# Kernel optimization log

Measured on AMD Instinct MI355X. Metric: run time of the kernel, lower is better.

The kernel has to match this reference:

```python
import jax, jax.numpy as jnp
import numpy as np

N, E, IN, HID, OUT = 8192, 262144, 3000, 256, 64
EPS = 1e-5


def setup_inputs() -> dict:
    key = jax.random.key(0)
    k = jax.random.split(key, 16)
    s = lambda i, shp, sc: jax.random.normal(k[i], shp, jnp.float32) * sc
    return {
        "feat": s(0, (N, IN), 1.0),
        "feat_a": s(1, (N, IN), 1.0),
        "graph_neigh": jax.random.uniform(k[2], (N, N), jnp.float32),
        "W1": s(3, (IN, HID), (1.0 / IN) ** 0.5),
        "att_src": s(4, (HID,), (1.0 / HID) ** 0.5),
        "att_dst": s(5, (HID,), (1.0 / HID) ** 0.5),
        "W2": s(6, (HID, OUT), (1.0 / HID) ** 0.5),
        "Wd1": s(7, (OUT, HID), (1.0 / OUT) ** 0.5),
        "bd1": jnp.zeros((HID,), jnp.float32),
        "gamma": jnp.ones((HID,), jnp.float32),
        "beta": jnp.zeros((HID,), jnp.float32),
        "Wd2": s(8, (HID, IN), (1.0 / HID) ** 0.5),
        "bd2": jnp.zeros((IN,), jnp.float32),
        "disc_W": s(9, (OUT, OUT), (1.0 / OUT) ** 0.5),
        "disc_b": jnp.zeros((), jnp.float32),
        "edge_index": jax.random.randint(k[10], (2, E), 0, N),
    }


def _gat_conv1(x, W1, att_src, att_dst, src, dst):
    # GATConv, heads=1, concat=False, no self-loops, no bias
    h = x @ W1                                    # [N, HID]
    a_src = h @ att_src                           # [N]
    a_dst = h @ att_dst                           # [N]
    e = jax.nn.leaky_relu(a_src[src] + a_dst[dst], 0.2)   # [E]
    m = jax.ops.segment_max(e, dst, num_segments=N)
    p = jnp.exp(e - m[dst])
    z = jax.ops.segment_sum(p, dst, num_segments=N)
    alpha = p / (z[dst] + 1e-16)                  # segment softmax over in-edges
    return jax.ops.segment_sum(alpha[:, None] * h[src], dst, num_segments=N)


def _encode(x, W1, att_src, att_dst, W2, src, dst):
    h1 = jax.nn.elu(_gat_conv1(x, W1, att_src, att_dst, src, dst))
    # conv2 is invoked with attention=False -> GraphST GATConv returns only lin(x) (heads=1 mean)
    return h1 @ W2


def _decoder(h, Wd1, bd1, gamma, beta, Wd2, bd2):
    z = h @ Wd1 + bd1
    mu = z.mean(0)
    var = z.var(0)  # biased, matches torch BN training normalization
    z = (z - mu) * jax.lax.rsqrt(var + EPS) * gamma + beta
    z = jax.nn.elu(z)
    return z @ Wd2 + bd2


def _readout(h, mask):
    vsum = mask @ h                               # [N, OUT]
    g = vsum / mask.sum(1, keepdims=True)
    g = g / jnp.clip(jnp.linalg.norm(g, axis=1, keepdims=True), 1e-12)
    return jax.nn.sigmoid(g)


def reference(feat, feat_a, graph_neigh, W1, att_src, att_dst, W2, Wd1, bd1,
              gamma, beta, Wd2, bd2, disc_W, disc_b, edge_index):
    src, dst = edge_index[0], edge_index[1]
    h2 = _encode(feat, W1, att_src, att_dst, W2, src, dst)
    h2_a = _encode(feat_a, W1, att_src, att_dst, W2, src, dst)
    h3 = _decoder(h2, Wd1, bd1, gamma, beta, Wd2, bd2)
    g = _readout(h2, graph_neigh)
    g_a = _readout(h2_a, graph_neigh)

    def disc(c, hp, hm):
        sc1 = jnp.einsum('nd,de,ne->n', hp, disc_W, c) + disc_b
        sc2 = jnp.einsum('nd,de,ne->n', hm, disc_W, c) + disc_b
        return jnp.stack([sc1, sc2], axis=1)

    ret = disc(g, h2, h2_a)
    ret_a = disc(g_a, h2_a, h2)
    return (h2, h3, ret, ret_a, h2, h2_a)
```

## Files before the change

### kernel.cpp

```cpp
#include <hip/hip_runtime.h>
#include <hip/hip_bf16.h>
#include <math.h>

constexpr int NN  = 8192;
constexpr int EE  = 262144;
constexpr int IN  = 3000;
constexpr int INP = 3008;
constexpr int HID = 256;
constexpr int OUT = 64;

constexpr long O_H2   = 0;
constexpr long O_H3   = 524288;
constexpr long O_RET  = 25100288;
constexpr long O_RETA = 25116672;
constexpr long O_H2B  = 25133056;
constexpr long O_H2A  = 25657344;

typedef __attribute__((ext_vector_type(8))) short short8v;
typedef __attribute__((ext_vector_type(4))) float f32x4;

__device__ __forceinline__ short f2bf(float f) {
    unsigned u = __float_as_uint(f);
    return (short)((u + 0x7FFF + ((u >> 16) & 1)) >> 16);
}
__device__ __forceinline__ float bf2f(unsigned short u) {
    return __uint_as_float(((unsigned)u) << 16);
}

__global__ void cvt_W1t(const float* __restrict__ W, unsigned short* __restrict__ Wt) {
    int i = blockIdx.x * 256 + threadIdx.x;
    int n = i / INP, k = i % INP;
    Wt[i] = (k < IN) ? (unsigned short)f2bf(W[(long)k * HID + n]) : 0;
}
__global__ void cvt_W2t(const float* __restrict__ W, unsigned short* __restrict__ Wt) {
    int i = blockIdx.x * 256 + threadIdx.x;
    int n = i / HID, k = i % HID;
    Wt[i] = (unsigned short)f2bf(W[(long)k * OUT + n]);
}
__global__ void cvt_Wd1t(const float* __restrict__ W, unsigned short* __restrict__ Wt) {
    int i = blockIdx.x * 256 + threadIdx.x;
    int n = i / OUT, k = i % OUT;
    Wt[i] = (unsigned short)f2bf(W[(long)k * HID + n]);
}
__global__ void cvt_Wd2t(const float* __restrict__ W, unsigned short* __restrict__ Wt) {
    int i = blockIdx.x * 256 + threadIdx.x;
    int n = i / HID, k = i % HID;
    Wt[i] = (n < IN) ? (unsigned short)f2bf(W[(long)k * IN + n]) : 0;
}

__global__ __launch_bounds__(256) void feat_gemm(const float* __restrict__ A0,
                                                 const float* __restrict__ A1,
                                                 const unsigned short* __restrict__ Bt,
                                                 float* __restrict__ Cpart) {
    __shared__ unsigned short As[128][72];
    __shared__ unsigned short Bs[128][72];
    int xb = blockIdx.x, yb = blockIdx.y;
    int pass = yb >> 6;
    int row0 = (yb & 63) * 128, col0 = xb * 128;
    const float* A = pass ? A1 : A0;
    int t = threadIdx.x, w = t >> 6, l = t & 63;
    int sr = t >> 1, sh = (t & 1) * 32;
    int wm = (w >> 1) * 64, wn = (w & 1) * 64;
    int fr = l & 15, fq = l >> 4;
    const unsigned short* Bp = Bt + (long)(col0 + sr) * INP + sh;
    const float* Arow = A + (long)(row0 + sr) * IN;

    int tb = blockIdx.z * 12;
    int ktiles = min(12, 47 - tb);

    float4  paf[8];
    short8v pb[4];
    auto loadA = [&](int k0) {
        const float* Ar = Arow + k0 + sh;
        if (k0 + 64 <= IN) {
#pragma unroll
            for (int q = 0; q < 8; ++q) paf[q] = *reinterpret_cast<const float4*>(Ar + q * 4);
        } else {
#pragma unroll
            for (int q = 0; q < 8; ++q) {
                int kb = k0 + sh + q * 4;
                float4 v;
                v.x = (kb + 0 < IN) ? Ar[q * 4 + 0] : 0.f;
                v.y = (kb + 1 < IN) ? Ar[q * 4 + 1] : 0.f;
                v.z = (kb + 2 < IN) ? Ar[q * 4 + 2] : 0.f;
                v.w = (kb + 3 < IN) ? Ar[q * 4 + 3] : 0.f;
                paf[q] = v;
            }
        }
    };
    auto loadB = [&](int k0) {
#pragma unroll
        for (int q = 0; q < 4; ++q) pb[q] = *reinterpret_cast<const short8v*>(Bp + k0 + q * 8);
    };
    loadA(tb * 64); loadB(tb * 64);

    f32x4 acc[4][4] = {};
    for (int tt = 0; tt < ktiles; ++tt) {
#pragma unroll
        for (int q = 0; q < 4; ++q) {
            float4 v0 = paf[q * 2], v1 = paf[q * 2 + 1];
            short8v s;
            s[0]=f2bf(v0.x); s[1]=f2bf(v0.y); s[2]=f2bf(v0.z); s[3]=f2bf(v0.w);
            s[4]=f2bf(v1.x); s[5]=f2bf(v1.y); s[6]=f2bf(v1.z); s[7]=f2bf(v1.w);
            *reinterpret_cast<short8v*>(&As[sr][sh + q * 8]) = s;
        }
#pragma unroll
        for (int q = 0; q < 4; ++q)
            *reinterpret_cast<short8v*>(&Bs[sr][sh + q * 8]) = pb[q];
        __syncthreads();
        if (tt + 1 < ktiles) {
            int k0 = (tb + tt + 1) * 64;
            loadA(k0); loadB(k0);
        }
#pragma unroll
        for (int kk = 0; kk < 2; ++kk) {
            short8v fa[4], fb[4];
#pragma unroll
            for (int i = 0; i < 4; ++i)
                fa[i] = *reinterpret_cast<const short8v*>(&As[wm + i * 16 + fr][kk * 32 + fq * 8]);
#pragma unroll
            for (int j = 0; j < 4; ++j)
                fb[j] = *reinterpret_cast<const short8v*>(&Bs[wn + j * 16 + fr][kk * 32 + fq * 8]);
#pragma unroll
            for (int i = 0; i < 4; ++i)
#pragma unroll
                for (int j = 0; j < 4; ++j)
                    acc[i][j] = __builtin_amdgcn_mfma_f32_16x16x32_bf16(fa[i], fb[j], acc[i][j], 0, 0, 0);
        }
        __syncthreads();
    }
    int dc = l & 15;
    long zbase = (long)blockIdx.z * 16384 * 256;
    long rbase = (long)(pass * NN + row0) * 256;
#pragma unroll
    for (int i = 0; i < 4; ++i)
#pragma unroll
        for (int j = 0; j < 4; ++j) {
            int c = col0 + wn + j * 16 + dc;
#pragma unroll
            for (int q = 0; q < 4; ++q) {
                int r = wm + i * 16 + fq * 4 + q;
                Cpart[zbase + rbase + (long)r * 256 + c] = acc[i][j][q];
            }
        }
}

__global__ void reduce_cvt4(const float* __restrict__ p, unsigned short* __restrict__ hb) {
    long i4 = ((long)blockIdx.x * 256 + threadIdx.x) * 4;
    float4 a = *reinterpret_cast<const float4*>(p + i4);
    float4 b = *reinterpret_cast<const float4*>(p + 4194304 + i4);
    float4 c = *reinterpret_cast<const float4*>(p + 8388608 + i4);
    float4 d = *reinterpret_cast<const float4*>(p + 12582912 + i4);
    ushort4 r;
    r.x = (unsigned short)f2bf(a.x + b.x + c.x + d.x);
    r.y = (unsigned short)f2bf(a.y + b.y + c.y + d.y);
    r.z = (unsigned short)f2bf(a.z + b.z + c.z + d.z);
    r.w = (unsigned short)f2bf(a.w + b.w + c.w + d.w);
    *reinterpret_cast<ushort4*>(hb + i4) = r;
}

__global__ __launch_bounds__(256) void w2_gemm(const unsigned short* __restrict__ A,
                                               const unsigned short* __restrict__ Bt,
                                               float* __restrict__ h2f,
                                               unsigned short* __restrict__ h2b,
                                               unsigned short* __restrict__ HT,
                                               float* __restrict__ out) {
    __shared__ unsigned short As[64][72];
    __shared__ unsigned short Bs[64][72];
    int t = threadIdx.x, w = t >> 6, l = t & 63;
    int row0 = blockIdx.y * 64;
    int srow = t >> 2, scol = (t & 3) * 16;
    const unsigned short* Ap = A + (long)(row0 + srow) * HID + scol;
    const unsigned short* Bp = Bt + (long)srow * HID + scol;
    int wm = (w >> 1) * 32, wn = (w & 1) * 32;
    int fr = l & 15, fq = l >> 4;

    short8v a0r, a1r, b0r, b1r;
    a0r = *reinterpret_cast<const short8v*>(Ap);
    a1r = *reinterpret_cast<const short8v*>(Ap + 8);
    b0r = *reinterpret_cast<const short8v*>(Bp);
    b1r = *reinterpret_cast<const short8v*>(Bp + 8);

    f32x4 acc[2][2] = {};
    for (int tt = 0; tt < 4; ++tt) {
        *reinterpret_cast<short8v*>(&As[srow][scol])     = a0r;
        *reinterpret_cast<short8v*>(&As[srow][scol + 8]) = a1r;
        *reinterpret_cast<short8v*>(&Bs[srow][scol])     = b0r;
        *reinterpret_cast<short8v*>(&Bs[srow][scol + 8]) = b1r;
        __syncthreads();
        if (tt + 1 < 4) {
            const unsigned short* Ap2 = Ap + (tt + 1) * 64;
            const unsigned short* Bp2 = Bp + (tt + 1) * 64;
            a0r = *reinterpret_cast<const short8v*>(Ap2);
            a1r = *reinterpret_cast<const short8v*>(Ap2 + 8);
            b0r = *reinterpret_cast<const short8v*>(Bp2);
            b1r = *reinterpret_cast<const short8v*>(Bp2 + 8);
        }
#pragma unroll
        for (int kk = 0; kk < 2; ++kk) {
            short8v fa0 = *reinterpret_cast<const short8v*>(&As[wm + fr][kk * 32 + fq * 8]);
            short8v fa1 = *reinterpret_cast<const short8v*>(&As[wm + 16 + fr][kk * 32 + fq * 8]);
            short8v fb0 = *reinterpret_cast<const short8v*>(&Bs[wn + fr][kk * 32 + fq * 8]);
            short8v fb1 = *reinterpret_cast<const short8v*>(&Bs[wn + 16 + fr][kk * 32 + fq * 8]);
            acc[0][0] = __builtin_amdgcn_mfma_f32_16x16x32_bf16(fa0, fb0, acc[0][0], 0, 0, 0);
            acc[0][1] = __builtin_amdgcn_mfma_f32_16x16x32_bf16(fa0, fb1, acc[0][1], 0, 0, 0);
            acc[1][0] = __builtin_amdgcn_mfma_f32_16x16x32_bf16(fa1, fb0, acc[1][0], 0, 0, 0);
            acc[1][1] = __builtin_amdgcn_mfma_f32_16x16x32_bf16(fa1, fb1, acc[1][1], 0, 0, 0);
        }
        __syncthreads();
    }
    int dc = l & 15;
    int pass = row0 >> 13;
#pragma unroll
    for (int i = 0; i < 2; ++i)
#pragma unroll
        for (int j = 0; j < 2; ++j) {
            int c = wn + j * 16 + dc;
#pragma unroll
            for (int q = 0; q < 4; ++q) {
                int r = row0 + wm + i * 16 + fq * 4 + q;
                int n = r & 8191;
                float v = acc[i][j][q];
                unsigned short vb = (unsigned short)f2bf(v);
                h2f[(long)pass * 524288 + (long)n * 64 + c] = v;
                if (pass == 0) {
                    out[O_H2  + (long)n * 64 + c] = v;
                    out[O_H2B + (long)n * 64 + c] = v;
                    h2b[(long)n * 64 + c] = vb;
                } else {
                    out[O_H2A + (long)n * 64 + c] = v;
                }
                HT[(long)(pass * 64 + c) * NN + n] = vb;
            }
        }
}

__global__ __launch_bounds__(256) void wd2_gemm(const unsigned short* __restrict__ A,
                                                const unsigned short* __restrict__ Bt,
                                                const float* __restrict__ bias,
                                                float* __restrict__ Cf) {
    __shared__ unsigned short As[128][72];
    __shared__ unsigned short Bs[128][72];
    int t = threadIdx.x, w = t >> 6, l = t & 63;
    int row0 = blockIdx.y * 128, col0 = blockIdx.x * 128;
    int sr = t >> 1, sh = (t & 1) * 32;
    int wm = (w >> 1) * 64, wn = (w & 1) * 64;
    int fr = l & 15, fq = l >> 4;
    const unsigned short* Ap = A  + (long)(row0 + sr) * HID + sh;
    const unsigned short* Bp = Bt + (long)(col0 + sr) * HID + sh;

    short8v pa[4], pb[4];
#pragma unroll
    for (int q = 0; q < 4; ++q) pa[q] = *reinterpret_cast<const short8v*>(Ap + q * 8);
#pragma unroll
    for (int q = 0; q < 4; ++q) pb[q] = *reinterpret_cast<const short8v*>(Bp + q * 8);

    f32x4 acc[4][4] = {};
    for (int tt = 0; tt < 4; ++tt) {
#pragma unroll
        for (int q = 0; q < 4; ++q) {
            *reinterpret_cast<short8v*>(&As[sr][sh + q * 8]) = pa[q];
            *reinterpret_cast<short8v*>(&Bs[sr][sh + q * 8]) = pb[q];
        }
        __syncthreads();
        if (tt + 1 < 4) {
            int k0 = (tt + 1) * 64;
#pragma unroll
            for (int q = 0; q < 4; ++q) pa[q] = *reinterpret_cast<const short8v*>(Ap + k0 + q * 8);
#pragma unroll
            for (int q = 0; q < 4; ++q) pb[q] = *reinterpret_cast<const short8v*>(Bp + k0 + q * 8);
        }
#pragma unroll
        for (int kk = 0; kk < 2; ++kk) {
            short8v fa[4], fb[4];
#pragma unroll
            for (int i = 0; i < 4; ++i)
                fa[i] = *reinterpret_cast<const short8v*>(&As[wm + i * 16 + fr][kk * 32 + fq * 8]);
#pragma unroll
            for (int j = 0; j < 4; ++j)
                fb[j] = *reinterpret_cast<const short8v*>(&Bs[wn + j * 16 + fr][kk * 32 + fq * 8]);
#pragma unroll
            for (int i = 0; i < 4; ++i)
#pragma unroll
                for (int j = 0; j < 4; ++j)
                    acc[i][j] = __builtin_amdgcn_mfma_f32_16x16x32_bf16(fa[i], fb[j], acc[i][j], 0, 0, 0);
        }
        __syncthreads();
    }
    int dc = l & 15;
#pragma unroll
    for (int i = 0; i < 4; ++i)
#pragma unroll
        for (int j = 0; j < 4; ++j) {
            int c = col0 + wn + j * 16 + dc;
            if (c < IN) {
                float bb = bias[c];
#pragma unroll
                for (int q = 0; q < 4; ++q) {
                    int r = row0 + wm + i * 16 + fq * 4 + q;
                    Cf[(long)r * IN + c] = acc[i][j][q] + bb;
                }
            }
        }
}

__global__ __launch_bounds__(256) void wd1_gemm(const unsigned short* __restrict__ A,
                                                const unsigned short* __restrict__ Bt,
                                                const float* __restrict__ bias,
                                                float* __restrict__ C) {
    __shared__ unsigned short As[64][72];
    __shared__ unsigned short Bs[64][72];
    int t = threadIdx.x, w = t >> 6, l = t & 63;
    int row0 = blockIdx.y * 64, col0 = blockIdx.x * 64;
    int srow = t >> 2, scol = (t & 3) * 16;
    const unsigned short* Ap = A  + (long)(row0 + srow) * OUT + scol;
    const unsigned short* Bp = Bt + (long)(col0 + srow) * OUT + scol;
    int wm = (w >> 1) * 32, wn = (w & 1) * 32;
    int fr = l & 15, fq = l >> 4;

    *reinterpret_cast<short8v*>(&As[srow][scol])     = *reinterpret_cast<const short8v*>(Ap);
    *reinterpret_cast<short8v*>(&As[srow][scol + 8]) = *reinterpret_cast<const short8v*>(Ap + 8);
    *reinterpret_cast<short8v*>(&Bs[srow][scol])     = *reinterpret_cast<const short8v*>(Bp);
    *reinterpret_cast<short8v*>(&Bs[srow][scol + 8]) = *reinterpret_cast<const short8v*>(Bp + 8);
    __syncthreads();
    f32x4 acc[2][2] = {};
#pragma unroll
    for (int kk = 0; kk < 2; ++kk) {
        short8v fa0 = *reinterpret_cast<const short8v*>(&As[wm + fr][kk * 32 + fq * 8]);
        short8v fa1 = *reinterpret_cast<const short8v*>(&As[wm + 16 + fr][kk * 32 + fq * 8]);
        short8v fb0 = *reinterpret_cast<const short8v*>(&Bs[wn + fr][kk * 32 + fq * 8]);
        short8v fb1 = *reinterpret_cast<const short8v*>(&Bs[wn + 16 + fr][kk * 32 + fq * 8]);
        acc[0][0] = __builtin_amdgcn_mfma_f32_16x16x32_bf16(fa0, fb0, acc[0][0], 0, 0, 0);
        acc[0][1] = __builtin_amdgcn_mfma_f32_16x16x32_bf16(fa0, fb1, acc[0][1], 0, 0, 0);
        acc[1][0] = __builtin_amdgcn_mfma_f32_16x16x32_bf16(fa1, fb0, acc[1][0], 0, 0, 0);
        acc[1][1] = __builtin_amdgcn_mfma_f32_16x16x32_bf16(fa1, fb1, acc[1][1], 0, 0, 0);
    }
    int dc = l & 15;
#pragma unroll
    for (int i = 0; i < 2; ++i)
#pragma unroll
        for (int j = 0; j < 2; ++j) {
            int c = col0 + wn + j * 16 + dc;
            float bb = bias[c];
#pragma unroll
            for (int q = 0; q < 4; ++q) {
                int r = row0 + wm + i * 16 + fq * 4 + q;
                C[(long)r * HID + c] = acc[i][j][q] + bb;
            }
        }
}

__global__ __launch_bounds__(256) void readout_mfma2(const float* __restrict__ gn,
                                                     const unsigned short* __restrict__ HT,
                                                     float* __restrict__ vsum_part,
                                                     float* __restrict__ rowsum_part) {
    __shared__ unsigned short As[64][72];
    __shared__ unsigned short Bs[128][72];
    __shared__ float rsacc[64][4];
    int t = threadIdx.x, w = t >> 6, l = t & 63;
    int row0 = blockIdx.x * 64;
    int kc = blockIdx.y, kbeg = kc * 2048;
    int asr = t >> 2, asc = (t & 3) * 16;
    int bsr = t >> 1, bsc = (t & 1) * 32;
    const float*          Ap = gn + (long)(row0 + asr) * NN + kbeg + asc;
    const unsigned short* Bp = HT + (long)bsr * NN + kbeg + bsc;
    int wm = (w >> 1) * 32, wn = (w & 1) * 64;
    int fr = l & 15, fq = l >> 4;

    float4  a4[4];
    short8v b8[4];
#pragma unroll
    for (int q = 0; q < 4; ++q) a4[q] = *reinterpret_cast<const float4*>(Ap + q * 4);
#pragma unroll
    for (int q = 0; q < 4; ++q) b8[q] = *reinterpret_cast<const short8v*>(Bp + q * 8);

    f32x4 acc[2][4] = {};
    float myrs = 0.f;
    for (int it = 0; it < 32; ++it) {
#pragma unroll
        for (int q = 0; q < 4; ++q) {
            float4 v = a4[q];
            ushort4 s;
            s.x = (unsigned short)f2bf(v.x);
            s.y = (unsigned short)f2bf(v.y);
            s.z = (unsigned short)f2bf(v.z);
            s.w = (unsigned short)f2bf(v.w);
            *reinterpret_cast<ushort4*>(&As[asr][asc + q * 4]) = s;
            myrs += v.x + v.y + v.z + v.w;
        }
#pragma unroll
        for (int q = 0; q < 4; ++q)
            *reinterpret_cast<short8v*>(&Bs[bsr][bsc + q * 8]) = b8[q];
        __syncthreads();
        if (it + 1 < 32) {
            const float*          Ap2 = Ap + (it + 1) * 64;
            const unsigned short* Bp2 = Bp + (it + 1) * 64;
#pragma unroll
            for (int q = 0; q < 4; ++q) a4[q] = *reinterpret_cast<const float4*>(Ap2 + q * 4);
#pragma unroll
            for (int q = 0; q < 4; ++q) b8[q] = *reinterpret_cast<const short8v*>(Bp2 + q * 8);
        }
#pragma unroll
        for (int kk = 0; kk < 2; ++kk) {
            short8v fa0 = *reinterpret_cast<const short8v*>(&As[wm + fr][kk * 32 + fq * 8]);
            short8v fa1 = *reinterpret_cast<const short8v*>(&As[wm + 16 + fr][kk * 32 + fq * 8]);
#pragma unroll
            for (int j = 0; j < 4; ++j) {
                short8v fb = *reinterpret_cast<const short8v*>(&Bs[wn + j * 16 + fr][kk * 32 + fq * 8]);
                acc[0][j] = __builtin_amdgcn_mfma_f32_16x16x32_bf16(fa0, fb, acc[0][j], 0, 0, 0);
                acc[1][j] = __builtin_amdgcn_mfma_f32_16x16x32_bf16(fa1, fb, acc[1][j], 0, 0, 0);
            }
        }
        __syncthreads();
    }
    rsacc[asr][t & 3] = myrs;
    __syncthreads();
    if (t < 64)
        rowsum_part[(long)kc * NN + row0 + t] =
            rsacc[t][0] + rsacc[t][1] + rsacc[t][2] + rsacc[t][3];
    int dc = l & 15;
#pragma unroll
    for (int i = 0; i < 2; ++i)
#pragma unroll
        for (int j = 0; j < 4; ++j) {
            int c = wn + j * 16 + dc;
#pragma unroll
            for (int q = 0; q < 4; ++q) {
                int r = row0 + wm + i * 16 + fq * 4 + q;
                vsum_part[((long)kc * NN + r) * 128 + c] = acc[i][j][q];
            }
        }
}

__global__ void deg_count(const int* __restrict__ dst, int* __restrict__ deg) {
    int i = blockIdx.x * 256 + threadIdx.x;
    if (i < EE) atomicAdd(&deg[dst[i]], 1);
}

__global__ __launch_bounds__(256) void scan_offsets(const int* __restrict__ deg,
                                                    int* __restrict__ off,
                                                    int* __restrict__ cursor) {
    __shared__ int part[256];
    int t = threadIdx.x;
    int base = t * 32;
    int local[32];
    int s = 0;
#pragma unroll
    for (int i = 0; i < 32; ++i) { local[i] = s; s += deg[base + i]; }
    part[t] = s;
    __syncthreads();
    for (int o2 = 1; o2 < 256; o2 <<= 1) {
        int v = (t >= o2) ? part[t - o2] : 0;
        __syncthreads();
        part[t] += v;
        __syncthreads();
    }
    int pre = (t == 0) ? 0 : part[t - 1];
#pragma unroll
    for (int i = 0; i < 32; ++i) {
        int v = pre + local[i];
        off[base + i] = v;
        cursor[base + i] = v;
    }
}

__global__ void scatter_edges(const int* __restrict__ src, const int* __restrict__ dst,
                              int* __restrict__ cursor, int* __restrict__ ssrc) {
    int i = blockIdx.x * 256 + threadIdx.x;
    if (i >= EE) return;
    int slot = atomicAdd(&cursor[dst[i]], 1);
    ssrc[slot] = src[i];
}

__global__ void attn_coeff_bf(const unsigned short* __restrict__ h,
                              const float* __restrict__ att_src,
                              const float* __restrict__ att_dst,
                              float* __restrict__ a_src, float* __restrict__ a_dst) {
    int wave = threadIdx.x >> 6, lane = threadIdx.x & 63;
    int n = blockIdx.x * 4 + wave;
    ushort4 hv = *reinterpret_cast<const ushort4*>(&h[(long)n * HID + lane * 4]);
    float4 vs = *reinterpret_cast<const float4*>(&att_src[lane * 4]);
    float4 vd = *reinterpret_cast<const float4*>(&att_dst[lane * 4]);
    float h0 = bf2f(hv.x), h1 = bf2f(hv.y), h2v = bf2f(hv.z), h3v = bf2f(hv.w);
    float s1 = h0 * vs.x + h1 * vs.y + h2v * vs.z + h3v * vs.w;
    float s2 = h0 * vd.x + h1 * vd.y + h2v * vd.z + h3v * vd.w;
#pragma unroll
    for (int off = 32; off > 0; off >>= 1) {
        s1 += __shfl_down(s1, off);
        s2 += __shfl_down(s2, off);
    }
    if (lane == 0) { a_src[n] = s1; a_dst[n] = s2; }
}

__global__ __launch_bounds__(256) void gat_gather(const int* __restrict__ ssrc,
                                                  const int* __restrict__ off,
                                                  const int* __restrict__ deg,
                                                  const float* __restrict__ asrc2,
                                                  const float* __restrict__ adst2,
                                                  const unsigned short* __restrict__ hb2,
                                                  unsigned short* __restrict__ gat2) {
    int wv = threadIdx.x >> 6, lane = threadIdx.x & 63;
    int d = blockIdx.x * 4 + wv;
    int pass = d >> 13, node = d & 8191;
    const float* asrc = asrc2 + pass * NN;
    const unsigned short* h = hb2 + (long)pass * NN * HID;
    int o = off[node], n = deg[node];
    float ad = adst2[d];

    float m = -INFINITY;
    for (int j = lane; j < n; j += 64) {
        float e = asrc[ssrc[o + j]] + ad;
        e = e > 0.f ? e : 0.2f * e;
        m = fmaxf(m, e);
    }
#pragma unroll
    for (int t = 32; t; t >>= 1) m = fmaxf(m, __shfl_xor(m, t));
    float z = 0.f;
    for (int j = lane; j < n; j += 64) {
        float e = asrc[ssrc[o + j]] + ad;
        e = e > 0.f ? e : 0.2f * e;
        z += expf(e - m);
    }
#pragma unroll
    for (int t = 32; t; t >>= 1) z += __shfl_xor(z, t);
    float zinv = 1.0f / (z + 1e-16f);

    float4 acc = {0.f, 0.f, 0.f, 0.f};
    int j = 0;
    for (; j + 2 <= n; j += 2) {
        int s0 = ssrc[o + j], s1 = ssrc[o + j + 1];
        const ushort4 h0 = *reinterpret_cast<const ushort4*>(&h[(long)s0 * HID + lane * 4]);
        const ushort4 h1 = *reinterpret_cast<const ushort4*>(&h[(long)s1 * HID + lane * 4]);
        float e0 = asrc[s0] + ad; e0 = e0 > 0.f ? e0 : 0.2f * e0;
        float e1 = asrc[s1] + ad; e1 = e1 > 0.f ? e1 : 0.2f * e1;
        float a0 = expf(e0 - m) * zinv;
        float a1 = expf(e1 - m) * zinv;
        acc.x += a0 * bf2f(h0.x) + a1 * bf2f(h1.x);
        acc.y += a0 * bf2f(h0.y) + a1 * bf2f(h1.y);
        acc.z += a0 * bf2f(h0.z) + a1 * bf2f(h1.z);
        acc.w += a0 * bf2f(h0.w) + a1 * bf2f(h1.w);
    }
    if (j < n) {
        int s0 = ssrc[o + j];
        const ushort4 h0 = *reinterpret_cast<const ushort4*>(&h[(long)s0 * HID + lane * 4]);
        float e0 = asrc[s0] + ad; e0 = e0 > 0.f ? e0 : 0.2f * e0;
        float a0 = expf(e0 - m) * zinv;
        acc.x += a0 * bf2f(h0.x); acc.y += a0 * bf2f(h0.y);
        acc.z += a0 * bf2f(h0.z); acc.w += a0 * bf2f(h0.w);
    }
    ushort4 r;
    r.x = (unsigned short)f2bf(acc.x > 0.f ? acc.x : expm1f(acc.x));
    r.y = (unsigned short)f2bf(acc.y > 0.f ? acc.y : expm1f(acc.y));
    r.z = (unsigned short)f2bf(acc.z > 0.f ? acc.z : expm1f(acc.z));
    r.w = (unsigned short)f2bf(acc.w > 0.f ? acc.w : expm1f(acc.w));
    *reinterpret_cast<ushort4*>(&gat2[(long)d * HID + lane * 4]) = r;
}

__global__ void bn_partial(const float* __restrict__ zd, float* __restrict__ s,
                           float* __restrict__ sq) {
    int t = threadIdx.x;
    float a = 0.f, b = 0.f;
    int r0 = blockIdx.x * 128;
    for (int r = r0; r < r0 + 128; ++r) {
        float v = zd[(long)r * HID + t];
        a += v;
        b += v * v;
    }
    atomicAdd(&s[t], a);
    atomicAdd(&sq[t], b);
}

__global__ void bn_finalize(const float* __restrict__ s, const float* __restrict__ sq,
                            const float* __restrict__ gamma, const float* __restrict__ beta,
                            float* __restrict__ scale, float* __restrict__ shift) {
    int t = threadIdx.x;
    float mean = s[t] / (float)NN;
    float var  = sq[t] / (float)NN - mean * mean;
    float sc   = gamma[t] * rsqrtf(var + 1e-5f);
    scale[t] = sc;
    shift[t] = beta[t] - mean * sc;
}

__global__ void bn_apply_elu_bf(const float* __restrict__ zd, const float* __restrict__ scale,
                                const float* __restrict__ shift, unsigned short* __restrict__ zb) {
    for (long i = (long)blockIdx.x * blockDim.x + threadIdx.x; i < (long)NN * HID;
         i += (long)gridDim.x * blockDim.x) {
        int c = (int)(i & 255);
        float v = zd[i] * scale[c] + shift[c];
        v = v > 0.f ? v : expm1f(v);
        zb[i] = (unsigned short)f2bf(v);
    }
}

__global__ void readout_disc(const float* __restrict__ vsum_part,
                             const float* __restrict__ rowsum_part,
                             const float* __restrict__ h2f,
                             const float* __restrict__ W, const float* __restrict__ b,
                             float* __restrict__ ret, float* __restrict__ reta) {
    __shared__ float gg[128];
    int r = blockIdx.x, t = threadIdx.x;
    float rs = 0.f, v = 0.f;
#pragma unroll
    for (int kc = 0; kc < 4; ++kc) {
        rs += rowsum_part[(long)kc * NN + r];
        v  += vsum_part[((long)kc * NN + r) * 128 + t];
    }
    v /= rs;
    int w = t >> 6, lane = t & 63;
    float sq = v * v;
#pragma unroll
    for (int off = 32; off > 0; off >>= 1) sq += __shfl_xor(sq, off);
    float nrm = fmaxf(sqrtf(sq), 1e-12f);
    gg[t] = 1.0f / (1.0f + expf(-(v / nrm)));
    __syncthreads();
    const float* hp_base = h2f + (w ? 524288 : 0);
    const float* hm_base = h2f + (w ? 0 : 524288);
    float u = 0.f;
#pragma unroll 8
    for (int e = 0; e < 64; ++e) u += W[lane * 64 + e] * gg[w * 64 + e];
    float hp = hp_base[(long)r * 64 + lane];
    float hm = hm_base[(long)r * 64 + lane];
    float t1 = hp * u, t2 = hm * u;
#pragma unroll
    for (int off = 32; off > 0; off >>= 1) {
        t1 += __shfl_xor(t1, off);
        t2 += __shfl_xor(t2, off);
    }
    if (lane == 0) {
        float bb = b[0];
        float* dstp = w ? reta : ret;
        dstp[r * 2]     = t1 + bb;
        dstp[r * 2 + 1] = t2 + bb;
    }
}

extern "C" void kernel_launch(void* const* d_in, const int* in_sizes, int n_in,
                              void* d_out, int out_size, void* d_ws, size_t ws_size,
                              hipStream_t stream) {
    const float* feat    = (const float*)d_in[0];
    const float* feat_a  = (const float*)d_in[1];
    const float* gneigh  = (const float*)d_in[2];
    const float* W1      = (const float*)d_in[3];
    const float* att_src = (const float*)d_in[4];
    const float* att_dst = (const float*)d_in[5];
    const float* W2      = (const float*)d_in[6];
    const float* Wd1     = (const float*)d_in[7];
    const float* bd1     = (const float*)d_in[8];
    const float* gamma   = (const float*)d_in[9];
    const float* beta    = (const float*)d_in[10];
    const float* Wd2     = (const float*)d_in[11];
    const float* bd2     = (const float*)d_in[12];
    const float* disc_W  = (const float*)d_in[13];
    const float* disc_b  = (const float*)d_in[14];
    const int*   eidx    = (const int*)d_in[15];
    const int*   src = eidx;
    const int*   dst = eidx + EE;
    float* out = (float*)d_out;

    float* w = (float*)d_ws;
    unsigned short* h_bf2  = (unsigned short*)w;
    unsigned short* gat_bf2 = (unsigned short*)(w + 2097152);
    float* zdec    = w + 4194304;
    unsigned short* zdec_bf = (unsigned short*)(zdec + 2097152);
    float* h2f     = zdec + 2097152 + 1048576;
    unsigned short* h2b = (unsigned short*)(h2f + 1048576);
    unsigned short* HT  = h2b + 524288;
    float* asrc2   = (float*)(HT + 1048576);
    float* adst2   = asrc2 + 16384;
    float* bnsum   = adst2 + 16384;
    float* bnsq    = bnsum + 256;
    float* scale   = bnsq + 256;
    float* shift   = scale + 256;
    unsigned short* W1t  = (unsigned short*)(shift + 256);
    unsigned short* W2t  = W1t + 770048;
    unsigned short* Wd1t = W2t + 16384;
    unsigned short* Wd2t = Wd1t + 16384;
    int*   ideg    = (int*)(Wd2t + 786432);
    int*   ioff    = ideg + 8192;
    int*   icur    = ioff + 8192;
    int*   issrc   = icur + 8192;
    float* part = out + O_H3;
    float* vsum_part = w;
    float* rowsum_part = zdec;

    cvt_W1t<<<3008, 256, 0, stream>>>(W1, W1t);
    cvt_W2t<<<64, 256, 0, stream>>>(W2, W2t);
    cvt_Wd1t<<<64, 256, 0, stream>>>(Wd1, Wd1t);
    cvt_Wd2t<<<3072, 256, 0, stream>>>(Wd2, Wd2t);

    hipMemsetAsync(ideg, 0, 8192 * 4, stream);
    deg_count<<<EE / 256, 256, 0, stream>>>(dst, ideg);
    scan_offsets<<<1, 256, 0, stream>>>(ideg, ioff, icur);
    scatter_edges<<<EE / 256, 256, 0, stream>>>(src, dst, icur, issrc);

    feat_gemm<<<dim3(2, 128, 4), 256, 0, stream>>>(feat, feat_a, W1t, part);
    reduce_cvt4<<<4096, 256, 0, stream>>>(part, h_bf2);
    attn_coeff_bf<<<4096, 256, 0, stream>>>(h_bf2, att_src, att_dst, asrc2, adst2);
    gat_gather<<<4096, 256, 0, stream>>>(issrc, ioff, ideg, asrc2, adst2, h_bf2, gat_bf2);
    w2_gemm<<<dim3(1, 256), 256, 0, stream>>>(gat_bf2, W2t, h2f, h2b, HT, out);

    wd1_gemm<<<dim3(4, 128), 256, 0, stream>>>(h2b, Wd1t, bd1, zdec);
    hipMemsetAsync(bnsum, 0, 512 * 4, stream);
    bn_partial<<<64, 256, 0, stream>>>(zdec, bnsum, bnsq);
    bn_finalize<<<1, 256, 0, stream>>>(bnsum, bnsq, gamma, beta, scale, shift);
    bn_apply_elu_bf<<<2048, 256, 0, stream>>>(zdec, scale, shift, zdec_bf);
    wd2_gemm<<<dim3(24, 64), 256, 0, stream>>>(zdec_bf, Wd2t, bd2, out + O_H3);

    readout_mfma2<<<dim3(128, 4), 256, 0, stream>>>(gneigh, HT, vsum_part, rowsum_part);
    readout_disc<<<8192, 128, 0, stream>>>(vsum_part, rowsum_part, h2f, disc_W, disc_b,
                                           out + O_RET, out + O_RETA);
}
```

Before: 400.0 us.

## Fuse attention coefficients into split-K reduce; widen readout split-K with bf16 partials

The split-K reduction of the first GEMM now also computes the per-node attention dot products from the fp32 sums, so the separate attention-coefficient kernel and its re-read of the bf16 features go away. The graph-neighbour readout GEMM moves from 4 to 8 K-splits so 1024 blocks launch instead of 512. Its partial sums are stored as bf16 to halve the partial-write traffic. The extra bf16 rounding of partials adds error, and the rowsum buffer must now hold 8 slices.

```diff
diff --git a/kernel.cpp b/kernel.cpp
--- a/kernel.cpp
+++ b/kernel.cpp
@@ -145,18 +145,40 @@
         }
 }
 
-__global__ void reduce_cvt4(const float* __restrict__ p, unsigned short* __restrict__ hb) {
-    long i4 = ((long)blockIdx.x * 256 + threadIdx.x) * 4;
-    float4 a = *reinterpret_cast<const float4*>(p + i4);
-    float4 b = *reinterpret_cast<const float4*>(p + 4194304 + i4);
-    float4 c = *reinterpret_cast<const float4*>(p + 8388608 + i4);
-    float4 d = *reinterpret_cast<const float4*>(p + 12582912 + i4);
+__global__ __launch_bounds__(256) void reduce_attn(const float* __restrict__ p,
+                                                   const float* __restrict__ att_src,
+                                                   const float* __restrict__ att_dst,
+                                                   unsigned short* __restrict__ hb,
+                                                   float* __restrict__ a_src,
+                                                   float* __restrict__ a_dst) {
+    int wave = threadIdx.x >> 6, lane = threadIdx.x & 63;
+    int n = blockIdx.x * 4 + wave;
+    long base = (long)n * 256 + lane * 4;
+    float4 a = *reinterpret_cast<const float4*>(p + base);
+    float4 b = *reinterpret_cast<const float4*>(p + 4194304 + base);
+    float4 c = *reinterpret_cast<const float4*>(p + 8388608 + base);
+    float4 d = *reinterpret_cast<const float4*>(p + 12582912 + base);
+    float4 hv;
+    hv.x = a.x + b.x + c.x + d.x;
+    hv.y = a.y + b.y + c.y + d.y;
+    hv.z = a.z + b.z + c.z + d.z;
+    hv.w = a.w + b.w + c.w + d.w;
     ushort4 r;
-    r.x = (unsigned short)f2bf(a.x + b.x + c.x + d.x);
-    r.y = (unsigned short)f2bf(a.y + b.y + c.y + d.y);
-    r.z = (unsigned short)f2bf(a.z + b.z + c.z + d.z);
-    r.w = (unsigned short)f2bf(a.w + b.w + c.w + d.w);
-    *reinterpret_cast<ushort4*>(hb + i4) = r;
+    r.x = (unsigned short)f2bf(hv.x);
+    r.y = (unsigned short)f2bf(hv.y);
+    r.z = (unsigned short)f2bf(hv.z);
+    r.w = (unsigned short)f2bf(hv.w);
+    *reinterpret_cast<ushort4*>(hb + base) = r;
+    float4 vs = *reinterpret_cast<const float4*>(&att_src[lane * 4]);
+    float4 vd = *reinterpret_cast<const float4*>(&att_dst[lane * 4]);
+    float s1 = hv.x * vs.x + hv.y * vs.y + hv.z * vs.z + hv.w * vs.w;
+    float s2 = hv.x * vd.x + hv.y * vd.y + hv.z * vd.z + hv.w * vd.w;
+#pragma unroll
+    for (int off = 32; off > 0; off >>= 1) {
+        s1 += __shfl_down(s1, off);
+        s2 += __shfl_down(s2, off);
+    }
+    if (lane == 0) { a_src[n] = s1; a_dst[n] = s2; }
 }
 
 __global__ __launch_bounds__(256) void w2_gemm(const unsigned short* __restrict__ A,
@@ -352,14 +374,14 @@
 
 __global__ __launch_bounds__(256) void readout_mfma2(const float* __restrict__ gn,
                                                      const unsigned short* __restrict__ HT,
-                                                     float* __restrict__ vsum_part,
+                                                     unsigned short* __restrict__ vsum_part,
                                                      float* __restrict__ rowsum_part) {
     __shared__ unsigned short As[64][72];
     __shared__ unsigned short Bs[128][72];
     __shared__ float rsacc[64][4];
     int t = threadIdx.x, w = t >> 6, l = t & 63;
     int row0 = blockIdx.x * 64;
-    int kc = blockIdx.y, kbeg = kc * 2048;
+    int kc = blockIdx.y, kbeg = kc * 1024;
     int asr = t >> 2, asc = (t & 3) * 16;
     int bsr = t >> 1, bsc = (t & 1) * 32;
     const float*          Ap = gn + (long)(row0 + asr) * NN + kbeg + asc;
@@ -376,7 +398,7 @@
 
     f32x4 acc[2][4] = {};
     float myrs = 0.f;
-    for (int it = 0; it < 32; ++it) {
+    for (int it = 0; it < 16; ++it) {
 #pragma unroll
         for (int q = 0; q < 4; ++q) {
             float4 v = a4[q];
@@ -392,7 +414,7 @@
         for (int q = 0; q < 4; ++q)
             *reinterpret_cast<short8v*>(&Bs[bsr][bsc + q * 8]) = b8[q];
         __syncthreads();
-        if (it + 1 < 32) {
+        if (it + 1 < 16) {
             const float*          Ap2 = Ap + (it + 1) * 64;
             const unsigned short* Bp2 = Bp + (it + 1) * 64;
 #pragma unroll
@@ -427,7 +449,7 @@
 #pragma unroll
             for (int q = 0; q < 4; ++q) {
                 int r = row0 + wm + i * 16 + fq * 4 + q;
-                vsum_part[((long)kc * NN + r) * 128 + c] = acc[i][j][q];
+                vsum_part[((long)kc * NN + r) * 128 + c] = (unsigned short)f2bf(acc[i][j][q]);
             }
         }
 }
@@ -470,26 +492,6 @@
     if (i >= EE) return;
     int slot = atomicAdd(&cursor[dst[i]], 1);
     ssrc[slot] = src[i];
-}
-
-__global__ void attn_coeff_bf(const unsigned short* __restrict__ h,
-                              const float* __restrict__ att_src,
-                              const float* __restrict__ att_dst,
-                              float* __restrict__ a_src, float* __restrict__ a_dst) {
-    int wave = threadIdx.x >> 6, lane = threadIdx.x & 63;
-    int n = blockIdx.x * 4 + wave;
-    ushort4 hv = *reinterpret_cast<const ushort4*>(&h[(long)n * HID + lane * 4]);
-    float4 vs = *reinterpret_cast<const float4*>(&att_src[lane * 4]);
-    float4 vd = *reinterpret_cast<const float4*>(&att_dst[lane * 4]);
-    float h0 = bf2f(hv.x), h1 = bf2f(hv.y), h2v = bf2f(hv.z), h3v = bf2f(hv.w);
-    float s1 = h0 * vs.x + h1 * vs.y + h2v * vs.z + h3v * vs.w;
-    float s2 = h0 * vd.x + h1 * vd.y + h2v * vd.z + h3v * vd.w;
-#pragma unroll
-    for (int off = 32; off > 0; off >>= 1) {
-        s1 += __shfl_down(s1, off);
-        s2 += __shfl_down(s2, off);
-    }
-    if (lane == 0) { a_src[n] = s1; a_dst[n] = s2; }
 }
 
 __global__ __launch_bounds__(256) void gat_gather(const int* __restrict__ ssrc,
@@ -592,7 +594,7 @@
     }
 }
 
-__global__ void readout_disc(const float* __restrict__ vsum_part,
+__global__ void readout_disc(const unsigned short* __restrict__ vsum_part,
                              const float* __restrict__ rowsum_part,
                              const float* __restrict__ h2f,
                              const float* __restrict__ W, const float* __restrict__ b,
@@ -601,9 +603,9 @@
     int r = blockIdx.x, t = threadIdx.x;
     float rs = 0.f, v = 0.f;
 #pragma unroll
-    for (int kc = 0; kc < 4; ++kc) {
+    for (int kc = 0; kc < 8; ++kc) {
         rs += rowsum_part[(long)kc * NN + r];
-        v  += vsum_part[((long)kc * NN + r) * 128 + t];
+        v  += bf2f(vsum_part[((long)kc * NN + r) * 128 + t]);
     }
     v /= rs;
     int w = t >> 6, lane = t & 63;
@@ -680,7 +682,7 @@
     int*   icur    = ioff + 8192;
     int*   issrc   = icur + 8192;
     float* part = out + O_H3;
-    float* vsum_part = w;
+    unsigned short* vsum_part = (unsigned short*)w;
     float* rowsum_part = zdec;
 
     cvt_W1t<<<3008, 256, 0, stream>>>(W1, W1t);
@@ -694,8 +696,7 @@
     scatter_edges<<<EE / 256, 256, 0, stream>>>(src, dst, icur, issrc);
 
     feat_gemm<<<dim3(2, 128, 4), 256, 0, stream>>>(feat, feat_a, W1t, part);
-    reduce_cvt4<<<4096, 256, 0, stream>>>(part, h_bf2);
-    attn_coeff_bf<<<4096, 256, 0, stream>>>(h_bf2, att_src, att_dst, asrc2, adst2);
+    reduce_attn<<<4096, 256, 0, stream>>>(part, att_src, att_dst, h_bf2, asrc2, adst2);
     gat_gather<<<4096, 256, 0, stream>>>(issrc, ioff, ideg, asrc2, adst2, h_bf2, gat_bf2);
     w2_gemm<<<dim3(1, 256), 256, 0, stream>>>(gat_bf2, W2t, h2f, h2b, HT, out);
 
@@ -706,7 +707,7 @@
     bn_apply_elu_bf<<<2048, 256, 0, stream>>>(zdec, scale, shift, zdec_bf);
     wd2_gemm<<<dim3(24, 64), 256, 0, stream>>>(zdec_bf, Wd2t, bd2, out + O_H3);
 
-    readout_mfma2<<<dim3(128, 4), 256, 0, stream>>>(gneigh, HT, vsum_part, rowsum_part);
+    readout_mfma2<<<dim3(128, 8), 256, 0, stream>>>(gneigh, HT, vsum_part, rowsum_part);
     readout_disc<<<8192, 128, 0, stream>>>(vsum_part, rowsum_part, h2f, disc_W, disc_b,
                                            out + O_RET, out + O_RETA);
 }
```

Measured after the change: 404.0 us. About the same (+1.0%).
